# Kernel optimization log

Hardware: AMD Instinct MI355X
Metric: run time of the kernel (lower is better)

Reference implementation:

```python
import jax, jax.numpy as jnp
import numpy as np

B, T, N, H = 256, 256, 512, 512  # batch, seq_len, input_size, hidden_size_encoder


def setup_inputs() -> dict:
    key = jax.random.key(0)
    k = jax.random.split(key, 9)
    return {
        "input_data": jax.random.normal(k[0], (B, T, N), dtype=jnp.float32),
        # init_hidden uses xavier_normal on zeros -> random init; std ~ sqrt(2/(B+H))
        "h0": jax.random.normal(k[1], (B, H), dtype=jnp.float32) * 0.06,
        "c0": jax.random.normal(k[2], (B, H), dtype=jnp.float32) * 0.06,
        # attn Linear: in_features = 2H + T, out_features = 1
        "attn_w": jax.random.normal(k[3], (2 * H + T,), dtype=jnp.float32) * 0.02,
        "attn_b": jnp.zeros((), dtype=jnp.float32),
        # single-layer LSTM params (torch gate order: i, f, g, o)
        "w_ih": jax.random.normal(k[4], (4 * H, N), dtype=jnp.float32) * 0.02,
        "w_hh": jax.random.normal(k[5], (4 * H, H), dtype=jnp.float32) * 0.02,
        "b_ih": jax.random.normal(k[6], (4 * H,), dtype=jnp.float32) * 0.02,
        "b_hh": jax.random.normal(k[7], (4 * H,), dtype=jnp.float32) * 0.02,
    }


def reference(input_data, h0, c0, attn_w, attn_b, w_ih, w_hh, b_ih, b_hh):
    Bd, Td, Nd = input_data.shape
    Hd = h0.shape[-1]
    # split attn weight into h-, c-, and x-parts (same math as the concat+Linear)
    w_h, w_c, w_x = attn_w[:Hd], attn_w[Hd:2 * Hd], attn_w[2 * Hd:]
    # x-part of the attention logits is time-invariant: [B, N]
    proj_x = jnp.einsum('btn,t->bn', input_data, w_x)
    b_gate = b_ih + b_hh  # [4H]

    def step(carry, x_t):  # x_t: [B, N]
        h, c = carry
        # attention logits: broadcast h/c contribution over the N input series
        e = proj_x + (h @ w_h)[:, None] + (c @ w_c)[:, None] + attn_b  # [B, N]
        a = jax.nn.softmax(e, axis=1)  # softmax over input_size dim
        weighted = a * x_t  # [B, N]
        gates = weighted @ w_ih.T + h @ w_hh.T + b_gate  # [B, 4H]
        i_g, f_g, g_g, o_g = jnp.split(gates, 4, axis=1)
        i_g = jax.nn.sigmoid(i_g)
        f_g = jax.nn.sigmoid(f_g)
        g_g = jnp.tanh(g_g)
        o_g = jax.nn.sigmoid(o_g)
        c_new = f_g * c + i_g * g_g
        h_new = o_g * jnp.tanh(c_new)
        return (h_new, c_new), (a, h_new)

    xs = jnp.swapaxes(input_data, 0, 1)  # [T, B, N]
    _, (attn_seq, enc_seq) = jax.lax.scan(step, (h0, c0), xs)
    attentions = jnp.swapaxes(attn_seq, 0, 1)      # [B, T, N]
    input_encoded = jnp.swapaxes(enc_seq, 0, 1)    # [B, T, H]
    return attentions, input_encoded
```

## Files before the change

kernel.cpp:

```cpp
#include <hip/hip_runtime.h>

#define BB 256
#define TT 256
#define NN 512
#define HH 512

typedef short short8 __attribute__((ext_vector_type(8)));
typedef float f32x4 __attribute__((ext_vector_type(4)));
typedef unsigned long long u64;

static __device__ __forceinline__ ushort f2bf(float f) {
  uint b = __builtin_bit_cast(uint, f);
  b += 0x7FFFu + ((b >> 16) & 1u);
  return (ushort)(b >> 16);
}
static __device__ __forceinline__ uint pk2(float lo, float hi) {
  return (uint)f2bf(lo) | ((uint)f2bf(hi) << 16);
}
static __device__ __forceinline__ float sigm_(float x) {
  return 1.0f / (1.0f + exp2f(-1.4426950408889634f * x));
}
static __device__ __forceinline__ float tanh_(float x) {
  return 2.0f / (1.0f + exp2f(-2.8853900817779268f * x)) - 1.0f;
}

__global__ __launch_bounds__(256) void prep_kernel(
    const float* __restrict__ w_ih, const float* __restrict__ w_hh,
    const float* __restrict__ b_ih, const float* __restrict__ b_hh,
    const float* __restrict__ h0,
    ushort* __restrict__ W2, float* __restrict__ bgate,
    uint* __restrict__ hx16a, unsigned* __restrict__ bar) {
  int idx = blockIdx.x * 256 + threadIdx.x;
  if (idx < 2048 * 1024) {
    int row = idx >> 10;
    int k = idx & 1023;
    float v = (k < NN) ? w_ih[row * NN + k] : w_hh[row * HH + (k - NN)];
    W2[idx] = f2bf(v);
  }
  if (idx < 2048) bgate[idx] = b_ih[idx] + b_hh[idx];
  if (idx < BB * HH / 2) hx16a[idx] = pk2(h0[2 * idx], h0[2 * idx + 1]);
  if (idx < 16 * 64) bar[idx] = 0u;
}

__global__ __launch_bounds__(256) void attn_kernel(
    const float* __restrict__ x, const float* __restrict__ attn_w,
    float* __restrict__ a_out, ushort* __restrict__ ax) {
  __shared__ float wx[TT];
  __shared__ float as[NN];
  __shared__ float red[8];
  const int b = blockIdx.x;
  const int tid = threadIdx.x;
  wx[tid] = attn_w[2 * HH + tid];
  __syncthreads();

  const float* xb = x + (size_t)b * TT * NN;
  float p0 = 0.0f, p1 = 0.0f;
  for (int t = 0; t < TT; ++t) {
    float w = wx[t];
    p0 += xb[t * NN + tid] * w;
    p1 += xb[t * NN + 256 + tid] * w;
  }

  const int lane = tid & 63, wv = tid >> 6;
  float m = fmaxf(p0, p1);
  #pragma unroll
  for (int o = 32; o; o >>= 1) m = fmaxf(m, __shfl_xor(m, o));
  if (lane == 0) red[wv] = m;
  __syncthreads();
  m = fmaxf(fmaxf(red[0], red[1]), fmaxf(red[2], red[3]));
  float e0 = expf(p0 - m), e1 = expf(p1 - m);
  float s = e0 + e1;
  #pragma unroll
  for (int o = 32; o; o >>= 1) s += __shfl_xor(s, o);
  if (lane == 0) red[4 + wv] = s;
  __syncthreads();
  s = red[4] + red[5] + red[6] + red[7];
  float inv = 1.0f / s;
  float a0 = e0 * inv, a1 = e1 * inv;
  a_out[b * NN + tid] = a0;
  a_out[b * NN + 256 + tid] = a1;
  as[tid] = a0;
  as[tid + 256] = a1;
  __syncthreads();

  const float aa0 = as[tid * 2], aa1 = as[tid * 2 + 1];
  ushort* axb = ax + (size_t)b * TT * NN;
  for (int t = 0; t < TT; ++t) {
    const float2 xv = *(const float2*)(xb + t * NN + tid * 2);
    *(uint*)(axb + t * NN + tid * 2) = pk2(aa0 * xv.x, aa1 * xv.y);
  }
}

__global__ __launch_bounds__(256) void bcast_kernel(
    const float* __restrict__ a, float* __restrict__ attn_out) {
  const size_t idx = (size_t)blockIdx.x * 256 + threadIdx.x;
  const int n4 = (int)(idx & 127);
  const int t = (int)((idx >> 7) & 255);
  const int b = (int)(idx >> 15);
  const float4 v = *(const float4*)(a + b * NN + n4 * 4);
  *(float4*)(attn_out + (((size_t)b * TT + t) * NN + n4 * 4)) = v;
}

__global__ __launch_bounds__(512, 2) void lstm_persistent(
    const ushort* __restrict__ ax,
    const ushort* __restrict__ W2,
    const float* __restrict__ bgate,
    const float* __restrict__ c0,
    uint* __restrict__ hx16a, uint* __restrict__ hx16b,
    float* __restrict__ enc,
    unsigned* __restrict__ bar) {
  __shared__ ushort hx[16 * 1024];
  __shared__ unsigned warr;
  __shared__ unsigned step_flag;

  const int tid = threadIdx.x;
  const int lane = tid & 63;
  const int w = tid >> 6;
  const int bg = blockIdx.x & 15;
  const int jt = blockIdx.x >> 4;
  const int gb0 = bg * 16;
  unsigned* const barp = bar + bg * 64;

  if (tid == 0) { warr = 0u; step_flag = 0u; }

  f32x4 areg[32];
  {
    const int r = lane & 15;
    const int grow = (r & 3) * 512 + jt * 32 + w * 4 + (r >> 2);
    const ushort* wp = W2 + (size_t)grow * 1024 + ((lane >> 4) << 3);
    #pragma unroll
    for (int i = 0; i < 32; ++i) {
      areg[i] = *(const f32x4*)(wp + (i << 5));
      asm volatile("" : "+v"(areg[i]));
    }
  }

  const int srow = tid >> 5;
  const int sl = tid & 31;
  const int r7 = srow & 7;

  const int eb = lane & 15;
  const int kq = lane >> 4;
  const int ecol = jt * 32 + w * 4 + kq;
  const float bgi = bgate[ecol];
  const float bgf = bgate[512 + ecol];
  const float bgg = bgate[1024 + ecol];
  const float bgo = bgate[1536 + ecol];
  float c_reg = c0[(size_t)(gb0 + eb) * HH + ecol];

  const int bbase = (lane & 15) * 1024;
  const int br7 = (lane & 15) & 7;

  uint4 px0, px1;
  {
    const ushort* axp = ax + ((size_t)(gb0 + srow) * TT + 0) * NN;
    px0 = *(const uint4*)(axp + sl * 8);
    px1 = *(const uint4*)(axp + 256 + sl * 8);
  }

  for (int t = 0; t < TT; ++t) {
    const uint* hin = (t & 1) ? hx16b : hx16a;
    uint* hout = (t & 1) ? hx16a : hx16b;

    *(uint4*)&hx[srow * 1024 + ((sl ^ r7) << 3)] = px0;
    *(uint4*)&hx[srow * 1024 + (((32 + sl) ^ r7) << 3)] = px1;
    if (t + 1 < TT) {
      const ushort* axp = ax + ((size_t)(gb0 + srow) * TT + (t + 1)) * NN;
      px0 = *(const uint4*)(axp + sl * 8);
      px1 = *(const uint4*)(axp + 256 + sl * 8);
    }
    __syncthreads();

    if (t && w == 0) {
      if (lane == 0) {
        const unsigned target = 16u * (unsigned)t;
        while (__hip_atomic_load(barp, __ATOMIC_RELAXED,
                                 __HIP_MEMORY_SCOPE_AGENT) < target)
          __builtin_amdgcn_s_sleep(1);
        __hip_atomic_store(&step_flag, (unsigned)t, __ATOMIC_RELEASE,
                           __HIP_MEMORY_SCOPE_WORKGROUP);
      }
    }

    f32x4 acc = {0.f, 0.f, 0.f, 0.f};
    #pragma unroll
    for (int ks = 0; ks < 16; ++ks) {
      const int ag = ks * 4 + kq;
      const short8 bf = *(const short8*)&hx[bbase + ((ag ^ br7) << 3)];
      acc = __builtin_amdgcn_mfma_f32_16x16x32_bf16(
          __builtin_bit_cast(short8, areg[ks]), bf, acc, 0, 0, 0);
    }

    if (t && w != 0) {
      if (lane == 0) {
        while (__hip_atomic_load(&step_flag, __ATOMIC_ACQUIRE,
                                 __HIP_MEMORY_SCOPE_WORKGROUP) < (unsigned)t) {}
      }
    }
    asm volatile("" ::: "memory");

    {
      const uint* hrow = hin + (size_t)(gb0 + srow) * 256;
      const u64 q0 = __hip_atomic_load((const u64*)(hrow + sl * 4),
                                       __ATOMIC_RELAXED, __HIP_MEMORY_SCOPE_AGENT);
      const u64 q1 = __hip_atomic_load((const u64*)(hrow + sl * 4 + 2),
                                       __ATOMIC_RELAXED, __HIP_MEMORY_SCOPE_AGENT);
      const u64 q2 = __hip_atomic_load((const u64*)(hrow + 128 + sl * 4),
                                       __ATOMIC_RELAXED, __HIP_MEMORY_SCOPE_AGENT);
      const u64 q3 = __hip_atomic_load((const u64*)(hrow + 128 + sl * 4 + 2),
                                       __ATOMIC_RELAXED, __HIP_MEMORY_SCOPE_AGENT);
      uint4 p0, p1;
      p0.x = (uint)q0; p0.y = (uint)(q0 >> 32);
      p0.z = (uint)q1; p0.w = (uint)(q1 >> 32);
      p1.x = (uint)q2; p1.y = (uint)(q2 >> 32);
      p1.z = (uint)q3; p1.w = (uint)(q3 >> 32);
      *(uint4*)&hx[srow * 1024 + (((64 + sl) ^ r7) << 3)] = p0;
      *(uint4*)&hx[srow * 1024 + (((96 + sl) ^ r7) << 3)] = p1;
    }
    __syncthreads();

    #pragma unroll
    for (int ks = 16; ks < 32; ++ks) {
      const int ag = ks * 4 + kq;
      const short8 bf = *(const short8*)&hx[bbase + ((ag ^ br7) << 3)];
      acc = __builtin_amdgcn_mfma_f32_16x16x32_bf16(
          __builtin_bit_cast(short8, areg[ks]), bf, acc, 0, 0, 0);
    }

    {
      const float ig = sigm_(acc[0] + bgi);
      const float fg = sigm_(acc[1] + bgf);
      const float gg = tanh_(acc[2] + bgg);
      const float og = sigm_(acc[3] + bgo);
      const float cn = fg * c_reg + ig * gg;
      const float hn = og * tanh_(cn);
      c_reg = cn;
      const float hp_ = __shfl_xor(hn, 16);
      if (!(lane & 16)) {
        __hip_atomic_store(hout + (size_t)(gb0 + eb) * 256 + (ecol >> 1),
                           pk2(hn, hp_),
                           __ATOMIC_RELAXED, __HIP_MEMORY_SCOPE_AGENT);
      }
      asm volatile("s_waitcnt vmcnt(0)" ::: "memory");
      if (lane == 0) {
        const unsigned old = __hip_atomic_fetch_add(
            &warr, 1u, __ATOMIC_ACQ_REL, __HIP_MEMORY_SCOPE_WORKGROUP);
        if (old == 8u * (unsigned)t + 7u)
          __hip_atomic_fetch_add(barp, 1u, __ATOMIC_RELAXED,
                                 __HIP_MEMORY_SCOPE_AGENT);
      }
      enc[((size_t)(gb0 + eb) * TT + t) * HH + ecol] = hn;
    }
  }
}

extern "C" void kernel_launch(void* const* d_in, const int* in_sizes, int n_in,
                              void* d_out, int out_size, void* d_ws, size_t ws_size,
                              hipStream_t stream) {
  const float* x      = (const float*)d_in[0];
  const float* h0     = (const float*)d_in[1];
  const float* c0     = (const float*)d_in[2];
  const float* attn_w = (const float*)d_in[3];
  const float* w_ih   = (const float*)d_in[5];
  const float* w_hh   = (const float*)d_in[6];
  const float* b_ih   = (const float*)d_in[7];
  const float* b_hh   = (const float*)d_in[8];

  float* attn_out = (float*)d_out;
  float* enc_out  = (float*)d_out + (size_t)BB * TT * NN;
  ushort* ax = (ushort*)d_out;

  char* ws = (char*)d_ws;
  float*    a_ws  = (float*)(ws);
  ushort*   W2_ws = (ushort*)(ws + 0x80000);
  float*    bg_ws = (float*)(ws + 0x480000);
  uint*     hx16a = (uint*)(ws + 0x482000);
  uint*     hx16b = (uint*)(ws + 0x4C2000);
  unsigned* bar   = (unsigned*)(ws + 0x502000);

  prep_kernel<<<8192, 256, 0, stream>>>(w_ih, w_hh, b_ih, b_hh, h0,
                                        W2_ws, bg_ws, hx16a, bar);
  attn_kernel<<<BB, 256, 0, stream>>>(x, attn_w, a_ws, ax);

  {
    dim3 grid(256), block(512);
    void* args[] = {(void*)&ax, (void*)&W2_ws, (void*)&bg_ws, (void*)&c0,
                    (void*)&hx16a, (void*)&hx16b, (void*)&enc_out,
                    (void*)&bar};
    hipLaunchCooperativeKernel((void*)lstm_persistent, grid, block, args, 0,
                               stream);
  }

  bcast_kernel<<<32768, 256, 0, stream>>>(a_ws, attn_out);
}
```

Measured before the change: 855.2 us.

## Replace counter barrier with step-tagged hidden-state words for inter-block sync

```diff
diff --git a/kernel.cpp b/kernel.cpp
--- a/kernel.cpp
+++ b/kernel.cpp
@@ -22,6 +22,10 @@
 }
 static __device__ __forceinline__ float tanh_(float x) {
   return 2.0f / (1.0f + exp2f(-2.8853900817779268f * x)) - 1.0f;
+}
+static __device__ __forceinline__ void bar_lds() {
+  asm volatile("s_waitcnt lgkmcnt(0)" ::: "memory");
+  __builtin_amdgcn_s_barrier();
 }
 
 __global__ __launch_bounds__(256) void prep_kernel(
@@ -29,7 +33,7 @@
     const float* __restrict__ b_ih, const float* __restrict__ b_hh,
     const float* __restrict__ h0,
     ushort* __restrict__ W2, float* __restrict__ bgate,
-    uint* __restrict__ hx16a, unsigned* __restrict__ bar) {
+    u64* __restrict__ hs1) {
   int idx = blockIdx.x * 256 + threadIdx.x;
   if (idx < 2048 * 1024) {
     int row = idx >> 10;
@@ -38,8 +42,8 @@
     W2[idx] = f2bf(v);
   }
   if (idx < 2048) bgate[idx] = b_ih[idx] + b_hh[idx];
-  if (idx < BB * HH / 2) hx16a[idx] = pk2(h0[2 * idx], h0[2 * idx + 1]);
-  if (idx < 16 * 64) bar[idx] = 0u;
+  if (idx < BB * HH / 2)
+    hs1[idx] = (u64)pk2(h0[2 * idx], h0[2 * idx + 1]);
 }
 
 __global__ __launch_bounds__(256) void attn_kernel(
@@ -106,12 +110,10 @@
     const ushort* __restrict__ W2,
     const float* __restrict__ bgate,
     const float* __restrict__ c0,
-    uint* __restrict__ hx16a, uint* __restrict__ hx16b,
-    float* __restrict__ enc,
-    unsigned* __restrict__ bar) {
+    u64* __restrict__ hs0,
+    u64* __restrict__ hs1,
+    float* __restrict__ enc) {
   __shared__ ushort hx[16 * 1024];
-  __shared__ unsigned warr;
-  __shared__ unsigned step_flag;
 
   const int tid = threadIdx.x;
   const int lane = tid & 63;
@@ -119,9 +121,6 @@
   const int bg = blockIdx.x & 15;
   const int jt = blockIdx.x >> 4;
   const int gb0 = bg * 16;
-  unsigned* const barp = bar + bg * 64;
-
-  if (tid == 0) { warr = 0u; step_flag = 0u; }
 
   f32x4 areg[32];
   {
@@ -151,6 +150,9 @@
   const int bbase = (lane & 15) * 1024;
   const int br7 = (lane & 15) & 7;
 
+  const size_t crow = (size_t)(gb0 + srow) * 256 + sl * 4;
+  const size_t pword = (size_t)(gb0 + eb) * 256 + (ecol >> 1);
+
   uint4 px0, px1;
   {
     const ushort* axp = ax + ((size_t)(gb0 + srow) * TT + 0) * NN;
@@ -159,8 +161,9 @@
   }
 
   for (int t = 0; t < TT; ++t) {
-    const uint* hin = (t & 1) ? hx16b : hx16a;
-    uint* hout = (t & 1) ? hx16a : hx16b;
+    const u64* hin = (((t + 1) & 1) ? hs1 : hs0) + crow;
+    u64* hout = ((t & 1) ? hs1 : hs0) + pword;
+    const uint exptag = (uint)t;
 
     *(uint4*)&hx[srow * 1024 + ((sl ^ r7) << 3)] = px0;
     *(uint4*)&hx[srow * 1024 + (((32 + sl) ^ r7) << 3)] = px1;
@@ -169,18 +172,17 @@
       px0 = *(const uint4*)(axp + sl * 8);
       px1 = *(const uint4*)(axp + 256 + sl * 8);
     }
-    __syncthreads();
-
-    if (t && w == 0) {
-      if (lane == 0) {
-        const unsigned target = 16u * (unsigned)t;
-        while (__hip_atomic_load(barp, __ATOMIC_RELAXED,
-                                 __HIP_MEMORY_SCOPE_AGENT) < target)
-          __builtin_amdgcn_s_sleep(1);
-        __hip_atomic_store(&step_flag, (unsigned)t, __ATOMIC_RELEASE,
-                           __HIP_MEMORY_SCOPE_WORKGROUP);
-      }
-    }
+    bar_lds();
+
+    u64 v[8];
+    #pragma unroll
+    for (int i = 0; i < 4; ++i)
+      v[i] = __hip_atomic_load(hin + i, __ATOMIC_RELAXED,
+                               __HIP_MEMORY_SCOPE_AGENT);
+    #pragma unroll
+    for (int i = 0; i < 4; ++i)
+      v[4 + i] = __hip_atomic_load(hin + 128 + i, __ATOMIC_RELAXED,
+                                   __HIP_MEMORY_SCOPE_AGENT);
 
     f32x4 acc = {0.f, 0.f, 0.f, 0.f};
     #pragma unroll
@@ -191,33 +193,34 @@
           __builtin_bit_cast(short8, areg[ks]), bf, acc, 0, 0, 0);
     }
 
-    if (t && w != 0) {
-      if (lane == 0) {
-        while (__hip_atomic_load(&step_flag, __ATOMIC_ACQUIRE,
-                                 __HIP_MEMORY_SCOPE_WORKGROUP) < (unsigned)t) {}
+    {
+      int spins = 0;
+      for (;;) {
+        uint ok = 1;
+        #pragma unroll
+        for (int i = 0; i < 8; ++i) ok &= ((uint)(v[i] >> 32) == exptag);
+        if (ok) break;
+        if (++spins > (1 << 18)) break;
+        __builtin_amdgcn_s_sleep(1);
+        #pragma unroll
+        for (int i = 0; i < 4; ++i)
+          v[i] = __hip_atomic_load(hin + i, __ATOMIC_RELAXED,
+                                   __HIP_MEMORY_SCOPE_AGENT);
+        #pragma unroll
+        for (int i = 0; i < 4; ++i)
+          v[4 + i] = __hip_atomic_load(hin + 128 + i, __ATOMIC_RELAXED,
+                                       __HIP_MEMORY_SCOPE_AGENT);
       }
     }
-    asm volatile("" ::: "memory");
 
     {
-      const uint* hrow = hin + (size_t)(gb0 + srow) * 256;
-      const u64 q0 = __hip_atomic_load((const u64*)(hrow + sl * 4),
-                                       __ATOMIC_RELAXED, __HIP_MEMORY_SCOPE_AGENT);
-      const u64 q1 = __hip_atomic_load((const u64*)(hrow + sl * 4 + 2),
-                                       __ATOMIC_RELAXED, __HIP_MEMORY_SCOPE_AGENT);
-      const u64 q2 = __hip_atomic_load((const u64*)(hrow + 128 + sl * 4),
-                                       __ATOMIC_RELAXED, __HIP_MEMORY_SCOPE_AGENT);
-      const u64 q3 = __hip_atomic_load((const u64*)(hrow + 128 + sl * 4 + 2),
-                                       __ATOMIC_RELAXED, __HIP_MEMORY_SCOPE_AGENT);
       uint4 p0, p1;
-      p0.x = (uint)q0; p0.y = (uint)(q0 >> 32);
-      p0.z = (uint)q1; p0.w = (uint)(q1 >> 32);
-      p1.x = (uint)q2; p1.y = (uint)(q2 >> 32);
-      p1.z = (uint)q3; p1.w = (uint)(q3 >> 32);
+      p0.x = (uint)v[0]; p0.y = (uint)v[1]; p0.z = (uint)v[2]; p0.w = (uint)v[3];
+      p1.x = (uint)v[4]; p1.y = (uint)v[5]; p1.z = (uint)v[6]; p1.w = (uint)v[7];
       *(uint4*)&hx[srow * 1024 + (((64 + sl) ^ r7) << 3)] = p0;
       *(uint4*)&hx[srow * 1024 + (((96 + sl) ^ r7) << 3)] = p1;
     }
-    __syncthreads();
+    bar_lds();
 
     #pragma unroll
     for (int ks = 16; ks < 32; ++ks) {
@@ -237,17 +240,9 @@
       c_reg = cn;
       const float hp_ = __shfl_xor(hn, 16);
       if (!(lane & 16)) {
-        __hip_atomic_store(hout + (size_t)(gb0 + eb) * 256 + (ecol >> 1),
-                           pk2(hn, hp_),
-                           __ATOMIC_RELAXED, __HIP_MEMORY_SCOPE_AGENT);
-      }
-      asm volatile("s_waitcnt vmcnt(0)" ::: "memory");
-      if (lane == 0) {
-        const unsigned old = __hip_atomic_fetch_add(
-            &warr, 1u, __ATOMIC_ACQ_REL, __HIP_MEMORY_SCOPE_WORKGROUP);
-        if (old == 8u * (unsigned)t + 7u)
-          __hip_atomic_fetch_add(barp, 1u, __ATOMIC_RELAXED,
-                                 __HIP_MEMORY_SCOPE_AGENT);
+        const u64 word = ((u64)(uint)(t + 1) << 32) | (u64)pk2(hn, hp_);
+        __hip_atomic_store(hout, word, __ATOMIC_RELAXED,
+                           __HIP_MEMORY_SCOPE_AGENT);
       }
       enc[((size_t)(gb0 + eb) * TT + t) * HH + ecol] = hn;
     }
@@ -271,22 +266,20 @@
   ushort* ax = (ushort*)d_out;
 
   char* ws = (char*)d_ws;
-  float*    a_ws  = (float*)(ws);
-  ushort*   W2_ws = (ushort*)(ws + 0x80000);
-  float*    bg_ws = (float*)(ws + 0x480000);
-  uint*     hx16a = (uint*)(ws + 0x482000);
-  uint*     hx16b = (uint*)(ws + 0x4C2000);
-  unsigned* bar   = (unsigned*)(ws + 0x502000);
+  float*  a_ws  = (float*)(ws);
+  ushort* W2_ws = (ushort*)(ws + 0x80000);
+  float*  bg_ws = (float*)(ws + 0x480000);
+  u64*    hs0   = (u64*)(ws + 0x482000);
+  u64*    hs1   = (u64*)(ws + 0x502000);
 
   prep_kernel<<<8192, 256, 0, stream>>>(w_ih, w_hh, b_ih, b_hh, h0,
-                                        W2_ws, bg_ws, hx16a, bar);
+                                        W2_ws, bg_ws, hs1);
   attn_kernel<<<BB, 256, 0, stream>>>(x, attn_w, a_ws, ax);
 
   {
     dim3 grid(256), block(512);
     void* args[] = {(void*)&ax, (void*)&W2_ws, (void*)&bg_ws, (void*)&c0,
-                    (void*)&hx16a, (void*)&hx16b, (void*)&enc_out,
-                    (void*)&bar};
+                    (void*)&hs0, (void*)&hs1, (void*)&enc_out};
     hipLaunchCooperativeKernel((void*)lstm_persistent, grid, block, args, 0,
                                stream);
   }
```

Result: slower. 1.196 ms (+39.9%).
